# Optimization experiments

Measured on AMD Instinct MI355X. Metric: run time of the kernel, lower is better.

The kernel has to match this reference:

```python
import jax, jax.numpy as jnp
import numpy as np

GROUPS = 8
HEADS = 8
EPS = 1e-5


def setup_inputs() -> dict:
    key = jax.random.key(0)
    ks = jax.random.split(key, 4)
    B, C, T = 4, 512, 2048
    x = jax.random.normal(ks[0], (B, C, T), dtype=jnp.float32)
    gn_w = jnp.ones((C,), dtype=jnp.float32)
    gn_b = jnp.zeros((C,), dtype=jnp.float32)
    qkv_w = jax.random.normal(ks[1], (3 * C, C), dtype=jnp.float32) * (1.0 / np.sqrt(C))
    qkv_b = jnp.zeros((3 * C,), dtype=jnp.float32)
    proj_w = jax.random.normal(ks[2], (C, C), dtype=jnp.float32) * (1.0 / np.sqrt(C))
    proj_b = jnp.zeros((C,), dtype=jnp.float32)
    return {"x": x, "gn_w": gn_w, "gn_b": gn_b, "qkv_w": qkv_w,
            "qkv_b": qkv_b, "proj_w": proj_w, "proj_b": proj_b}


def reference(x, gn_w, gn_b, qkv_w, qkv_b, proj_w, proj_b):
    b, c, t = x.shape
    # GroupNorm over (channels_in_group, T)
    xg = x.reshape(b, GROUPS, c // GROUPS, t)
    mean = xg.mean(axis=(2, 3), keepdims=True)
    var = xg.var(axis=(2, 3), keepdims=True)
    h = ((xg - mean) * jax.lax.rsqrt(var + EPS)).reshape(b, c, t)
    h = h * gn_w[None, :, None] + gn_b[None, :, None]
    # 1x1 conv qkv: [b, 3c, t]
    qkv = jnp.einsum('oc,bct->bot', qkv_w, h) + qkv_b[None, :, None]
    # split into heads: legacy layout [b*H, 3*ch, t] -> q,k,v each [b*H, ch, t]
    ch = c // HEADS
    qkv = qkv.reshape(b * HEADS, 3 * ch, t)
    q, k, v = qkv[:, :ch], qkv[:, ch:2 * ch], qkv[:, 2 * ch:]
    scale = 1.0 / np.sqrt(np.sqrt(ch))
    weight = jnp.einsum('bct,bcs->bts', q * scale, k * scale)  # [bH, t, t]
    weight = jax.nn.softmax(weight.astype(jnp.float32), axis=-1).astype(q.dtype)
    a = jnp.einsum('bts,bcs->bct', weight, v).reshape(b, c, t)
    # 1x1 conv proj
    out = jnp.einsum('oc,bct->bot', proj_w, a) + proj_b[None, :, None]
    return x + out
```

## Files before the change

### kernel.cpp

```cpp
#include <hip/hip_runtime.h>


typedef __attribute__((ext_vector_type(8))) short short8;
typedef __attribute__((ext_vector_type(4))) float f32x4;
typedef __attribute__((ext_vector_type(16))) float f32x16;

#define T_DIM 2048
#define C_DIM 512
#define B_DIM 4

__device__ __forceinline__ float bf2f(ushort u) {
  union { unsigned int i; float f; } x; x.i = ((unsigned int)u) << 16; return x.f;
}
__device__ __forceinline__ ushort f2bf(float f) {
  union { float f; unsigned int i; } x; x.f = f;
  unsigned int i = x.i;
  return (ushort)((i + 0x7FFFu + ((i >> 16) & 1u)) >> 16);
}
__device__ __forceinline__ unsigned int cvtpk_bf16(float lo, float hi) {
  unsigned int r;
  asm("v_cvt_pk_bf16_f32 %0, %1, %2" : "=v"(r) : "v"(lo), "v"(hi));
  return r;
}
__device__ __forceinline__ float exp2_raw(float x) {
  float r;
  asm("v_exp_f32 %0, %1" : "=v"(r) : "v"(x));
  return r;
}
__device__ __forceinline__ void gl_lds16(const ushort* g, const ushort* l) {
  __builtin_amdgcn_global_load_lds(
      (const __attribute__((address_space(1))) unsigned int*)g,
      (__attribute__((address_space(3))) unsigned int*)l, 16, 0, 0);
}

__global__ __launch_bounds__(256) void prep_kernel(
    const float* __restrict__ qkv_w, ushort* __restrict__ wq,
    const float* __restrict__ proj_w, ushort* __restrict__ wp,
    const float* __restrict__ x, float2* __restrict__ part) {
  const int bi = blockIdx.x;
  const int tid = threadIdx.x;
  if (bi < 1024) {
    const float* s = (bi < 768) ? qkv_w : proj_w;
    ushort* d = (bi < 768) ? wq : wp;
    int i = ((bi < 768) ? bi : bi - 768) * 256 + tid;
    float4 v = ((const float4*)s)[i];
    ushort4 o;
    o.x = f2bf(v.x); o.y = f2bf(v.y); o.z = f2bf(v.z); o.w = f2bf(v.w);
    ((ushort4*)d)[i] = o;
    return;
  }
  const int pb = bi - 1024;
  const float4* p4 = (const float4*)x + (size_t)pb * 2048;
  float s = 0.f, ss = 0.f;
#pragma unroll
  for (int i = 0; i < 8; i++) {
    float4 v = p4[tid + i * 256];
    s += v.x + v.y + v.z + v.w;
    ss += v.x * v.x + v.y * v.y + v.z * v.z + v.w * v.w;
  }
  for (int off = 32; off; off >>= 1) {
    s += __shfl_xor(s, off, 64);
    ss += __shfl_xor(ss, off, 64);
  }
  __shared__ float rbuf[8];
  int w = tid >> 6, lane = tid & 63;
  if (lane == 0) { rbuf[w * 2] = s; rbuf[w * 2 + 1] = ss; }
  __syncthreads();
  if (tid == 0) {
    float S = 0.f, SS = 0.f;
#pragma unroll
    for (int i = 0; i < 4; i++) { S += rbuf[2 * i]; SS += rbuf[2 * i + 1]; }
    part[pb] = make_float2(S, SS);
  }
}

__global__ __launch_bounds__(256) void gn_apply_t_kernel(
    const float* __restrict__ x, const float* __restrict__ gw,
    const float* __restrict__ gb, const float2* __restrict__ part,
    ushort* __restrict__ ht) {
  __shared__ ushort tile[64][66];
  __shared__ float sst[2];
  const int b = blockIdx.z, gy = blockIdx.y, c0 = gy * 64, t0 = blockIdx.x * 64;
  const int tid = threadIdx.x;
  if (tid < 64) {
    float s = 0.f, ss = 0.f;
    if (tid < 16) {
      float2 p = part[(b * 8 + gy) * 16 + tid];
      s = p.x; ss = p.y;
    }
    for (int off = 8; off; off >>= 1) {
      s += __shfl_xor(s, off, 64);
      ss += __shfl_xor(ss, off, 64);
    }
    if (tid == 0) {
      float mean = s * (1.f / 131072.f);
      float var = ss * (1.f / 131072.f) - mean * mean;
      sst[0] = mean;
      sst[1] = rsqrtf(var + 1e-5f);
    }
  }
  __syncthreads();
  const float mean = sst[0], rstd = sst[1];
  {
    const int cc = tid >> 2, tc = (tid & 3) * 16;
    const int c = c0 + cc;
    float sc = rstd * gw[c];
    float bb = gb[c] - mean * sc;
    const float4* src = (const float4*)(x + ((size_t)b * 512 + c) * T_DIM + t0 + tc);
    unsigned int* dst = (unsigned int*)&tile[cc][tc];
#pragma unroll
    for (int q = 0; q < 4; q++) {
      float4 v = src[q];
      float a0 = v.x * sc + bb, a1 = v.y * sc + bb;
      float a2 = v.z * sc + bb, a3 = v.w * sc + bb;
      dst[2 * q] = (unsigned int)f2bf(a0) | ((unsigned int)f2bf(a1) << 16);
      dst[2 * q + 1] = (unsigned int)f2bf(a2) | ((unsigned int)f2bf(a3) << 16);
    }
  }
  __syncthreads();
  {
    const int tt = tid >> 2, ch = (tid & 3) * 16;
    union { uint4 v4[2]; ushort u[16]; } z;
#pragma unroll
    for (int j = 0; j < 16; j++) z.u[j] = tile[ch + j][tt];
    ushort* dst = ht + ((size_t)b * T_DIM + t0 + tt) * 512 + c0 + ch;
    *(uint4*)dst = z.v4[0];
    *(uint4*)(dst + 8) = z.v4[1];
  }
}

template <int MODE>
__global__ __launch_bounds__(256, 3) void gemm_bt_kernel(
    const ushort* __restrict__ Wb, const ushort* __restrict__ Bt,
    const float* __restrict__ bias, const float* __restrict__ xres,
    ushort* __restrict__ outb, float* __restrict__ outf, int M) {
  __shared__ ushort As[128 * 64];
  __shared__ ushort Bs[128 * 64];
  const int b = blockIdx.z;
  const int t0 = blockIdx.x * 128, o0 = blockIdx.y * 128;
  const int tid = threadIdx.x, lane = tid & 63, w = tid >> 6;
  const int li = lane & 15, g = lane >> 4;
  const int wm = (w >> 1) * 64, wn = (w & 1) * 64;
  const int r8 = tid >> 3, bl = tid & 7;
  const ushort* Bbase = Bt + (size_t)b * T_DIM * 512;

  f32x4 acc[4][4];
#pragma unroll
  for (int m = 0; m < 4; m++)
#pragma unroll
    for (int n = 0; n < 4; n++) acc[m][n] = (f32x4){0.f, 0.f, 0.f, 0.f};

  for (int ks = 0; ks < 8; ks++) {
    const int k0 = ks * 64;
#pragma unroll
    for (int i = 0; i < 4; i++) {
      int row = i * 32 + r8;
      int sb = (bl ^ (row & 7)) << 3;
      gl_lds16(Wb + (size_t)(o0 + row) * 512 + k0 + sb, As + row * 64 + bl * 8);
      gl_lds16(Bbase + (size_t)(t0 + row) * 512 + k0 + sb, Bs + row * 64 + bl * 8);
    }
    __syncthreads();
#pragma unroll
    for (int kk = 0; kk < 2; kk++) {
      short8 af[4], bf[4];
#pragma unroll
      for (int m = 0; m < 4; m++)
        af[m] = *(const short8*)&As[(wm + m * 16 + li) * 64 +
                                    (((kk * 4 + g) ^ (li & 7)) << 3)];
#pragma unroll
      for (int n = 0; n < 4; n++)
        bf[n] = *(const short8*)&Bs[(wn + n * 16 + li) * 64 +
                                    (((kk * 4 + g) ^ (li & 7)) << 3)];
      __builtin_amdgcn_s_setprio(1);
#pragma unroll
      for (int m = 0; m < 4; m++)
#pragma unroll
        for (int n = 0; n < 4; n++)
          acc[m][n] = __builtin_amdgcn_mfma_f32_16x16x32_bf16(af[m], bf[n],
                                                              acc[m][n], 0, 0, 0);
      __builtin_amdgcn_s_setprio(0);
    }
    __syncthreads();
  }

  size_t obase = (size_t)b * M * T_DIM;
#pragma unroll
  for (int m = 0; m < 4; m++) {
#pragma unroll
    for (int r = 0; r < 4; r++) {
      int o = o0 + wm + m * 16 + g * 4 + r;
      float bv = bias[o];
#pragma unroll
      for (int n = 0; n < 4; n++) {
        int t = t0 + wn + n * 16 + li;
        float v = acc[m][n][r] + bv;
        size_t idx = obase + (size_t)o * T_DIM + t;
        if (MODE == 0) outb[idx] = f2bf(v);
        else outf[idx] = v + xres[idx];
      }
    }
  }
}

__global__ __launch_bounds__(256) void transk_kernel(
    const ushort* __restrict__ qkv, ushort* __restrict__ Kt) {
  __shared__ ushort tile[64][72];
  const int tb = blockIdx.x, bh = blockIdx.y, b = bh >> 3, hh = bh & 7;
  const ushort* src = qkv + ((size_t)b * 1536 + hh * 192 + 64) * T_DIM + tb * 64;
  const int tid = threadIdx.x;
  {
    int d = tid >> 2, tc = (tid & 3) * 16;
    union { uint4 v; ushort u[8]; } x0, x1, y0, y1;
    x0.v = *(const uint4*)(src + (size_t)d * T_DIM + tc);
    x1.v = *(const uint4*)(src + (size_t)d * T_DIM + tc + 8);
#pragma unroll
    for (int j = 0; j < 8; j++) {
      y0.u[j] = f2bf(0.1803368801f * bf2f(x0.u[j]));
      y1.u[j] = f2bf(0.1803368801f * bf2f(x1.u[j]));
    }
    *(uint4*)&tile[d][tc] = y0.v;
    *(uint4*)&tile[d][tc + 8] = y1.v;
  }
  __syncthreads();
  {
    int tt = tid & 63, c0 = (tid >> 6) * 16;
    union { uint4 v; ushort u[8]; } z0, z1;
#pragma unroll
    for (int j = 0; j < 8; j++) {
      z0.u[j] = tile[c0 + j][tt];
      z1.u[j] = tile[c0 + 8 + j][tt];
    }
    ushort* dst = Kt + ((size_t)bh * T_DIM + tb * 64 + tt) * 64 + c0;
    *(uint4*)dst = z0.v;
    *(uint4*)(dst + 8) = z1.v;
  }
}

__global__ __launch_bounds__(256, 4) void attn_part_kernel(
    const ushort* __restrict__ qkv, const ushort* __restrict__ Ktg,
    ushort* __restrict__ opart, float* __restrict__ lpart) {
  __shared__ ushort SH[16384];
  const int bh = blockIdx.x, b = bh >> 3, hh = bh & 7;
  const int ttile = blockIdx.y;
  const int t0 = ttile * 128;
  const int shalf = blockIdx.z;
  const int tid = threadIdx.x, lane = tid & 63, w = tid >> 6;
  const int tl = lane & 31, hi = lane >> 5;
  const size_t base = ((size_t)b * 1536 + hh * 192) * (size_t)T_DIM;
  const ushort* Qp = qkv + base;
  const ushort* Vp = qkv + base + (size_t)128 * T_DIM + shalf * 1024;
  const ushort* Kp = Ktg + (size_t)bh * T_DIM * 64 + (size_t)shalf * 1024 * 64;
  const int tcol = t0 + w * 32 + tl;

  short8 qb[4];
#pragma unroll
  for (int kc = 0; kc < 4; kc++) {
    union { short8 s; ushort u[8]; } tmp;
#pragma unroll
    for (int j = 0; j < 8; j++)
      tmp.u[j] = Qp[(size_t)(kc * 16 + hi * 8 + j) * T_DIM + tcol];
    qb[kc] = tmp.s;
  }

  const int srow = lane >> 3;
  const int sblk = (lane & 7) ^ srow;

  const ushort* kg = Kp + (size_t)(w * 16 + srow) * 64 + sblk * 8;
  const ushort* vg = Vp + (size_t)(w * 16 + srow) * T_DIM + sblk * 8;
  const int ldW = w * 1024;

  f32x16 zv;
#pragma unroll
  for (int r = 0; r < 16; r++) zv[r] = 0.f;
  f32x16 oacc0, oacc1;
#pragma unroll
  for (int r = 0; r < 16; r++) { oacc0[r] = 0.f; oacc1[r] = 0.f; }
  float lsum = 0.f;

  gl_lds16(kg, SH + ldW);
  gl_lds16(kg + 512, SH + ldW + 512);
  gl_lds16(vg, SH + 8192 + ldW);
  gl_lds16(vg + 8 * T_DIM, SH + 8192 + ldW + 512);
  kg += 4096;
  vg += 64;

#define CHUNK(BUF, PF)                                                        \
  {                                                                           \
    __syncthreads();                                                          \
    if (PF) {                                                                 \
      gl_lds16(kg, SH + ((BUF) ^ 1) * 4096 + ldW);                            \
      gl_lds16(kg + 512, SH + ((BUF) ^ 1) * 4096 + ldW + 512);                \
      gl_lds16(vg, SH + 8192 + ((BUF) ^ 1) * 4096 + ldW);                     \
      gl_lds16(vg + 8 * T_DIM, SH + 8192 + ((BUF) ^ 1) * 4096 + ldW + 512);   \
      kg += 4096;                                                             \
      vg += 64;                                                               \
    }                                                                         \
    const ushort* kb = SH + (BUF) * 4096;                                     \
    const ushort* vb = SH + 8192 + (BUF) * 4096;                              \
    f32x16 s0, s1;                                                            \
    __builtin_amdgcn_s_setprio(1);                                            \
    _Pragma("unroll") for (int kc = 0; kc < 4; kc++) {                        \
      const int bo = (((kc * 2 + hi) ^ (tl & 7)) << 3);                       \
      short8 ak0 = *(const short8*)&kb[tl * 64 + bo];                         \
      short8 ak1 = *(const short8*)&kb[(32 + tl) * 64 + bo];                  \
      s0 = __builtin_amdgcn_mfma_f32_32x32x16_bf16(ak0, qb[kc],               \
                                                   kc == 0 ? zv : s0, 0, 0, 0);\
      s1 = __builtin_amdgcn_mfma_f32_32x32x16_bf16(ak1, qb[kc],               \
                                                   kc == 0 ? zv : s1, 0, 0, 0);\
    }                                                                         \
    __builtin_amdgcn_s_setprio(0);                                            \
    _Pragma("unroll") for (int r = 0; r < 16; r++) {                          \
      s0[r] = exp2_raw(s0[r]);                                                \
      s1[r] = exp2_raw(s1[r]);                                                \
    }                                                                         \
    {                                                                         \
      float a0 = (s0[0] + s0[1]) + (s0[2] + s0[3]);                           \
      float a1 = (s0[4] + s0[5]) + (s0[6] + s0[7]);                           \
      float a2 = (s0[8] + s0[9]) + (s0[10] + s0[11]);                         \
      float a3 = (s0[12] + s0[13]) + (s0[14] + s0[15]);                       \
      float b0 = (s1[0] + s1[1]) + (s1[2] + s1[3]);                           \
      float b1 = (s1[4] + s1[5]) + (s1[6] + s1[7]);                           \
      float b2 = (s1[8] + s1[9]) + (s1[10] + s1[11]);                         \
      float b3 = (s1[12] + s1[13]) + (s1[14] + s1[15]);                       \
      lsum += ((a0 + a1) + (a2 + a3)) + ((b0 + b1) + (b2 + b3));              \
    }                                                                         \
    unsigned int pw[2][8];                                                    \
    _Pragma("unroll") for (int p = 0; p < 8; p++) {                           \
      pw[0][p] = cvtpk_bf16(s0[2 * p], s0[2 * p + 1]);                        \
      pw[1][p] = cvtpk_bf16(s1[2 * p], s1[2 * p + 1]);                        \
    }                                                                         \
    short8 bp[4];                                                             \
    _Pragma("unroll") for (int kc = 0; kc < 4; kc++) {                        \
      const int n = kc >> 1, q = (kc & 1) * 4;                                \
      union { short8 s; unsigned int wv[4]; } bu;                             \
      _Pragma("unroll") for (int h = 0; h < 2; h++) {                         \
        unsigned int P0 = pw[n][q + h];                                       \
        unsigned int P1 = pw[n][q + 2 + h];                                   \
        asm volatile("v_permlane32_swap_b32 %0, %1" : "+v"(P0), "+v"(P1));    \
        bu.wv[h] = P0;                                                        \
        bu.wv[2 + h] = P1;                                                    \
      }                                                                       \
      bp[kc] = bu.s;                                                          \
    }                                                                         \
    __builtin_amdgcn_s_setprio(1);                                            \
    _Pragma("unroll") for (int kc = 0; kc < 4; kc++) {                        \
      const int bo = (((kc * 2 + hi) ^ (tl & 7)) << 3);                       \
      short8 av0 = *(const short8*)&vb[tl * 64 + bo];                         \
      short8 av1 = *(const short8*)&vb[(32 + tl) * 64 + bo];                  \
      oacc0 = __builtin_amdgcn_mfma_f32_32x32x16_bf16(av0, bp[kc], oacc0,     \
                                                      0, 0, 0);               \
      oacc1 = __builtin_amdgcn_mfma_f32_32x32x16_bf16(av1, bp[kc], oacc1,     \
                                                      0, 0, 0);               \
    }                                                                         \
    __builtin_amdgcn_s_setprio(0);                                            \
  }

  for (int cc = 0; cc < 8; cc++) {
    CHUNK(0, true);
    CHUNK(1, cc < 7);
  }
#undef CHUNK

  const int pidx = (bh * 16 + ttile) * 2 + shalf;
  ushort* op = opart + (size_t)pidx * 8192;
#pragma unroll
  for (int r = 0; r < 16; r++) {
    int crow = (r & 3) + 8 * (r >> 2) + 4 * hi;
    op[crow * 128 + w * 32 + tl] = f2bf(oacc0[r]);
    op[(32 + crow) * 128 + w * 32 + tl] = f2bf(oacc1[r]);
  }
  float lrow = lsum + __shfl_xor(lsum, 32);
  if (hi == 0) lpart[(size_t)pidx * 128 + w * 32 + tl] = lrow;
}

__global__ __launch_bounds__(256) void combine_kernel(
    const ushort* __restrict__ opart, const float* __restrict__ lpart,
    ushort* __restrict__ at) {
  __shared__ float invl[128];
  __shared__ ushort tile[128][66];
  const int ttile = blockIdx.x, bh = blockIdx.y, b = bh >> 3, hh = bh & 7;
  const int tid = threadIdx.x;
  const size_t pb = (size_t)(bh * 16 + ttile) * 2;
  const float* l0 = lpart + pb * 128;
  if (tid < 128) invl[tid] = 1.f / (l0[tid] + l0[128 + tid]);
  __syncthreads();
  {
    const int c = tid & 63, seg = tid >> 6;
    const ushort* r0 = opart + pb * 8192 + c * 128 + seg * 32;
    union { uint4 v[4]; ushort u[32]; } x0, x1;
#pragma unroll
    for (int j = 0; j < 4; j++) {
      x0.v[j] = *(const uint4*)(r0 + j * 8);
      x1.v[j] = *(const uint4*)(r0 + 8192 + j * 8);
    }
#pragma unroll
    for (int j = 0; j < 32; j++) {
      int t = seg * 32 + j;
      tile[t][c] = f2bf((bf2f(x0.u[j]) + bf2f(x1.u[j])) * invl[t]);
    }
  }
  __syncthreads();
  {
    const int t = tid >> 1, ch = (tid & 1) * 32;
    union { uint4 v[4]; ushort u[32]; } z;
#pragma unroll
    for (int j = 0; j < 32; j++) z.u[j] = tile[t][ch + j];
    uint4* dst = (uint4*)(at + ((size_t)b * T_DIM + ttile * 128 + t) * 512 +
                          hh * 64 + ch);
#pragma unroll
    for (int j = 0; j < 4; j++) dst[j] = z.v[j];
  }
}

extern "C" void kernel_launch(void* const* d_in, const int* in_sizes, int n_in,
                              void* d_out, int out_size, void* d_ws,
                              size_t ws_size, hipStream_t stream) {
  const float* x = (const float*)d_in[0];
  const float* gn_w = (const float*)d_in[1];
  const float* gn_b = (const float*)d_in[2];
  const float* qkv_w = (const float*)d_in[3];
  const float* qkv_b = (const float*)d_in[4];
  const float* proj_w = (const float*)d_in[5];
  const float* proj_b = (const float*)d_in[6];
  float* out = (float*)d_out;

  char* ws = (char*)d_ws;
  float2* part = (float2*)ws;
  ushort* ht_bf = (ushort*)(ws + 8192);
  ushort* at_bf = ht_bf;
  ushort* qkv_bf = (ushort*)(ws + 8192 + 8388608);
  ushort* wq_bf = (ushort*)(ws + 8192 + 8388608 + 25165824);
  ushort* wp_bf = (ushort*)(ws + 8192 + 8388608 + 25165824 + 1572864);
  ushort* kt_bf = (ushort*)(ws + 8192 + 8388608 + 25165824 + 1572864 + 524288);
  ushort* op_bf = (ushort*)(ws + 8192 + 8388608 + 25165824 + 1572864 + 524288 +
                            8388608);
  float* lp_f = (float*)(ws + 8192 + 8388608 + 25165824 + 1572864 + 524288 +
                         8388608 + 16777216);

  prep_kernel<<<1536, 256, 0, stream>>>(qkv_w, wq_bf, proj_w, wp_bf, x, part);
  gn_apply_t_kernel<<<dim3(32, 8, 4), 256, 0, stream>>>(x, gn_w, gn_b, part, ht_bf);
  gemm_bt_kernel<0><<<dim3(16, 12, 4), 256, 0, stream>>>(
      wq_bf, ht_bf, qkv_b, nullptr, qkv_bf, nullptr, 1536);
  transk_kernel<<<dim3(32, 32), 256, 0, stream>>>(qkv_bf, kt_bf);
  attn_part_kernel<<<dim3(32, 16, 2), 256, 0, stream>>>(qkv_bf, kt_bf, op_bf, lp_f);
  combine_kernel<<<dim3(16, 32), 256, 0, stream>>>(op_bf, lp_f, at_bf);
  gemm_bt_kernel<1><<<dim3(16, 4, 4), 256, 0, stream>>>(
      wp_bf, at_bf, proj_b, x, nullptr, out, 512);
}
```

Before: 105.6 us.

## Fuse K transpose into QKV GEMM epilogue and split attention keys four ways

The QKV GEMM epilogue now writes the K rows directly into the transposed, pre-scaled Kt layout, so the separate transpose kernel is no longer launched. The attention kernel splits the key dimension into four quarters instead of two, doubling the grid to raise occupancy across CUs. The combine kernel sums four partials, and its grid axes are swapped. The trade-offs are more partial-output traffic and combine work, plus scattered 8-byte epilogue stores for K.

```diff
diff --git a/kernel.cpp b/kernel.cpp
--- a/kernel.cpp
+++ b/kernel.cpp
@@ -32,6 +32,8 @@
       (const __attribute__((address_space(1))) unsigned int*)g,
       (__attribute__((address_space(3))) unsigned int*)l, 16, 0, 0);
 }
+
+#define KT_SCALE 0.1803368801f
 
 __global__ __launch_bounds__(256) void prep_kernel(
     const float* __restrict__ qkv_w, ushort* __restrict__ wq,
@@ -133,7 +135,8 @@
 __global__ __launch_bounds__(256, 3) void gemm_bt_kernel(
     const ushort* __restrict__ Wb, const ushort* __restrict__ Bt,
     const float* __restrict__ bias, const float* __restrict__ xres,
-    ushort* __restrict__ outb, float* __restrict__ outf, int M) {
+    ushort* __restrict__ outb, float* __restrict__ outf,
+    ushort* __restrict__ ktp, int M) {
   __shared__ ushort As[128 * 64];
   __shared__ ushort Bs[128 * 64];
   const int b = blockIdx.z;
@@ -186,53 +189,46 @@
   size_t obase = (size_t)b * M * T_DIM;
 #pragma unroll
   for (int m = 0; m < 4; m++) {
-#pragma unroll
-    for (int r = 0; r < 4; r++) {
-      int o = o0 + wm + m * 16 + g * 4 + r;
-      float bv = bias[o];
+    const int om = o0 + wm + m * 16;
+    bool isK = false;
+    int head = 0, rem0 = 0;
+    if (MODE == 0) {
+      head = om / 192;
+      rem0 = om - head * 192;
+      isK = (rem0 >= 64 && rem0 < 128);
+    }
+    if (MODE == 0 && isK) {
+      const int d0 = rem0 - 64 + g * 4;
+      const size_t ktbase = (size_t)(b * 8 + head) * T_DIM;
+      float bv0 = bias[om + g * 4 + 0];
+      float bv1 = bias[om + g * 4 + 1];
+      float bv2 = bias[om + g * 4 + 2];
+      float bv3 = bias[om + g * 4 + 3];
 #pragma unroll
       for (int n = 0; n < 4; n++) {
         int t = t0 + wn + n * 16 + li;
-        float v = acc[m][n][r] + bv;
-        size_t idx = obase + (size_t)o * T_DIM + t;
-        if (MODE == 0) outb[idx] = f2bf(v);
-        else outf[idx] = v + xres[idx];
+        ushort4 kv;
+        kv.x = f2bf(KT_SCALE * (acc[m][n][0] + bv0));
+        kv.y = f2bf(KT_SCALE * (acc[m][n][1] + bv1));
+        kv.z = f2bf(KT_SCALE * (acc[m][n][2] + bv2));
+        kv.w = f2bf(KT_SCALE * (acc[m][n][3] + bv3));
+        *(ushort4*)(ktp + (ktbase + t) * 64 + d0) = kv;
       }
-    }
-  }
-}
-
-__global__ __launch_bounds__(256) void transk_kernel(
-    const ushort* __restrict__ qkv, ushort* __restrict__ Kt) {
-  __shared__ ushort tile[64][72];
-  const int tb = blockIdx.x, bh = blockIdx.y, b = bh >> 3, hh = bh & 7;
-  const ushort* src = qkv + ((size_t)b * 1536 + hh * 192 + 64) * T_DIM + tb * 64;
-  const int tid = threadIdx.x;
-  {
-    int d = tid >> 2, tc = (tid & 3) * 16;
-    union { uint4 v; ushort u[8]; } x0, x1, y0, y1;
-    x0.v = *(const uint4*)(src + (size_t)d * T_DIM + tc);
-    x1.v = *(const uint4*)(src + (size_t)d * T_DIM + tc + 8);
-#pragma unroll
-    for (int j = 0; j < 8; j++) {
-      y0.u[j] = f2bf(0.1803368801f * bf2f(x0.u[j]));
-      y1.u[j] = f2bf(0.1803368801f * bf2f(x1.u[j]));
-    }
-    *(uint4*)&tile[d][tc] = y0.v;
-    *(uint4*)&tile[d][tc + 8] = y1.v;
-  }
-  __syncthreads();
-  {
-    int tt = tid & 63, c0 = (tid >> 6) * 16;
-    union { uint4 v; ushort u[8]; } z0, z1;
-#pragma unroll
-    for (int j = 0; j < 8; j++) {
-      z0.u[j] = tile[c0 + j][tt];
-      z1.u[j] = tile[c0 + 8 + j][tt];
-    }
-    ushort* dst = Kt + ((size_t)bh * T_DIM + tb * 64 + tt) * 64 + c0;
-    *(uint4*)dst = z0.v;
-    *(uint4*)(dst + 8) = z1.v;
+    } else {
+#pragma unroll
+      for (int r = 0; r < 4; r++) {
+        int o = om + g * 4 + r;
+        float bv = bias[o];
+#pragma unroll
+        for (int n = 0; n < 4; n++) {
+          int t = t0 + wn + n * 16 + li;
+          float v = acc[m][n][r] + bv;
+          size_t idx = obase + (size_t)o * T_DIM + t;
+          if (MODE == 0) outb[idx] = f2bf(v);
+          else outf[idx] = v + xres[idx];
+        }
+      }
+    }
   }
 }
 
@@ -243,13 +239,13 @@
   const int bh = blockIdx.x, b = bh >> 3, hh = bh & 7;
   const int ttile = blockIdx.y;
   const int t0 = ttile * 128;
-  const int shalf = blockIdx.z;
+  const int sq = blockIdx.z;
   const int tid = threadIdx.x, lane = tid & 63, w = tid >> 6;
   const int tl = lane & 31, hi = lane >> 5;
   const size_t base = ((size_t)b * 1536 + hh * 192) * (size_t)T_DIM;
   const ushort* Qp = qkv + base;
-  const ushort* Vp = qkv + base + (size_t)128 * T_DIM + shalf * 1024;
-  const ushort* Kp = Ktg + (size_t)bh * T_DIM * 64 + (size_t)shalf * 1024 * 64;
+  const ushort* Vp = qkv + base + (size_t)128 * T_DIM + sq * 512;
+  const ushort* Kp = Ktg + (size_t)bh * T_DIM * 64 + (size_t)sq * 512 * 64;
   const int tcol = t0 + w * 32 + tl;
 
   short8 qb[4];
@@ -355,13 +351,13 @@
     __builtin_amdgcn_s_setprio(0);                                            \
   }
 
-  for (int cc = 0; cc < 8; cc++) {
+  for (int cc = 0; cc < 4; cc++) {
     CHUNK(0, true);
-    CHUNK(1, cc < 7);
+    CHUNK(1, cc < 3);
   }
 #undef CHUNK
 
-  const int pidx = (bh * 16 + ttile) * 2 + shalf;
+  const int pidx = (bh * 16 + ttile) * 4 + sq;
   ushort* op = opart + (size_t)pidx * 8192;
 #pragma unroll
   for (int r = 0; r < 16; r++) {
@@ -378,25 +374,29 @@
     ushort* __restrict__ at) {
   __shared__ float invl[128];
   __shared__ ushort tile[128][66];
-  const int ttile = blockIdx.x, bh = blockIdx.y, b = bh >> 3, hh = bh & 7;
+  const int bh = blockIdx.x, ttile = blockIdx.y, b = bh >> 3, hh = bh & 7;
   const int tid = threadIdx.x;
-  const size_t pb = (size_t)(bh * 16 + ttile) * 2;
+  const size_t pb = (size_t)(bh * 16 + ttile) * 4;
   const float* l0 = lpart + pb * 128;
-  if (tid < 128) invl[tid] = 1.f / (l0[tid] + l0[128 + tid]);
+  if (tid < 128)
+    invl[tid] = 1.f / (l0[tid] + l0[128 + tid] + l0[256 + tid] + l0[384 + tid]);
   __syncthreads();
   {
     const int c = tid & 63, seg = tid >> 6;
     const ushort* r0 = opart + pb * 8192 + c * 128 + seg * 32;
-    union { uint4 v[4]; ushort u[32]; } x0, x1;
+    union { uint4 v[4]; ushort u[32]; } x0, x1, x2, x3;
 #pragma unroll
     for (int j = 0; j < 4; j++) {
       x0.v[j] = *(const uint4*)(r0 + j * 8);
       x1.v[j] = *(const uint4*)(r0 + 8192 + j * 8);
+      x2.v[j] = *(const uint4*)(r0 + 16384 + j * 8);
+      x3.v[j] = *(const uint4*)(r0 + 24576 + j * 8);
     }
 #pragma unroll
     for (int j = 0; j < 32; j++) {
       int t = seg * 32 + j;
-      tile[t][c] = f2bf((bf2f(x0.u[j]) + bf2f(x1.u[j])) * invl[t]);
+      float v = (bf2f(x0.u[j]) + bf2f(x1.u[j])) + (bf2f(x2.u[j]) + bf2f(x3.u[j]));
+      tile[t][c] = f2bf(v * invl[t]);
     }
   }
   __syncthreads();
@@ -435,15 +435,14 @@
   ushort* op_bf = (ushort*)(ws + 8192 + 8388608 + 25165824 + 1572864 + 524288 +
                             8388608);
   float* lp_f = (float*)(ws + 8192 + 8388608 + 25165824 + 1572864 + 524288 +
-                         8388608 + 16777216);
+                         8388608 + 33554432);
 
   prep_kernel<<<1536, 256, 0, stream>>>(qkv_w, wq_bf, proj_w, wp_bf, x, part);
   gn_apply_t_kernel<<<dim3(32, 8, 4), 256, 0, stream>>>(x, gn_w, gn_b, part, ht_bf);
   gemm_bt_kernel<0><<<dim3(16, 12, 4), 256, 0, stream>>>(
-      wq_bf, ht_bf, qkv_b, nullptr, qkv_bf, nullptr, 1536);
-  transk_kernel<<<dim3(32, 32), 256, 0, stream>>>(qkv_bf, kt_bf);
-  attn_part_kernel<<<dim3(32, 16, 2), 256, 0, stream>>>(qkv_bf, kt_bf, op_bf, lp_f);
-  combine_kernel<<<dim3(16, 32), 256, 0, stream>>>(op_bf, lp_f, at_bf);
+      wq_bf, ht_bf, qkv_b, nullptr, qkv_bf, nullptr, kt_bf, 1536);
+  attn_part_kernel<<<dim3(32, 16, 4), 256, 0, stream>>>(qkv_bf, kt_bf, op_bf, lp_f);
+  combine_kernel<<<dim3(32, 16), 256, 0, stream>>>(op_bf, lp_f, at_bf);
   gemm_bt_kernel<1><<<dim3(16, 4, 4), 256, 0, stream>>>(
-      wp_bf, at_bf, proj_b, x, nullptr, out, 512);
-}
+      wp_bf, at_bf, proj_b, x, nullptr, out, nullptr, 512);
+}
```

Result: no change. 107.1 us (+1.4%).
